# Performance work log

Measured on AMD Instinct MI355X. Metric: run time of the kernel, lower is better.

Reference implementation:

```python
import jax, jax.numpy as jnp
import numpy as np

N, D = 16384, 256
T = 0.5
C = 100


def setup_inputs() -> dict:
    key = jax.random.key(0)
    x = jax.random.normal(key, (N, D), dtype=jnp.float32)
    # L2-normalize rows (standard for contrastive embeddings; also keeps
    # exp(sim/T) in fp32 range, matching the module's intended use)
    x = x / jnp.linalg.norm(x, axis=1, keepdims=True)
    return {"x": x}


def reference(x) -> jnp.ndarray:
    # sim[i,j] = <x_i, x_j> / T ; loss = (1/C) * sum_i log(sum_j exp(sim[i,j]))
    sim = jnp.exp(jnp.matmul(x, x.T) / T)          # [N, N]
    row = jnp.log(jnp.sum(sim, axis=1))            # [N]
    return jnp.sum(row) / C                        # scalar
```

## Files before the change

kernel.cpp:

```cpp
#include <hip/hip_runtime.h>
#include <hip/hip_bf16.h>
#include <math.h>


#define N_ROWS 16384
#define KD     256
#define BM     256
#define BN     64
#define NT     (N_ROWS / BM)
#define NITER  (BM / BN)
#define NBLK   (NT * (NT + 1) / 2)

#define SCALE_SQRT 1.6986436f

typedef short short8 __attribute__((ext_vector_type(8)));
typedef float f32x4  __attribute__((ext_vector_type(4)));

typedef __attribute__((address_space(3))) void       lds_void;
typedef const __attribute__((address_space(1))) void gm_void;

__device__ __forceinline__ float fast_exp2(float x) {
#if __has_builtin(__builtin_amdgcn_exp2f)
    return __builtin_amdgcn_exp2f(x);
#else
    return exp2f(x);
#endif
}

__device__ __forceinline__ void gll16(const void* g, void* l) {
    __builtin_amdgcn_global_load_lds((gm_void*)g, (lds_void*)l, 16, 0, 0);
}

__global__ void convert_kernel(const float* __restrict__ x, unsigned short* __restrict__ xb,
                               float* __restrict__ out) {
    const int bx = blockIdx.x, tid = threadIdx.x;
    if (bx == 0 && tid == 0) out[0] = 0.f;
    int i = (bx * 256 + tid) * 4;
    float4 v = *(const float4*)(x + i);
    ushort4 o;
    {
        unsigned int u;
        u = __float_as_uint(v.x * SCALE_SQRT); u += 0x7fff + ((u >> 16) & 1); o.x = (unsigned short)(u >> 16);
        u = __float_as_uint(v.y * SCALE_SQRT); u += 0x7fff + ((u >> 16) & 1); o.y = (unsigned short)(u >> 16);
        u = __float_as_uint(v.z * SCALE_SQRT); u += 0x7fff + ((u >> 16) & 1); o.z = (unsigned short)(u >> 16);
        u = __float_as_uint(v.w * SCALE_SQRT); u += 0x7fff + ((u >> 16) & 1); o.w = (unsigned short)(u >> 16);
    }
    *(ushort4*)(xb + i) = o;
}

__global__ __launch_bounds__(256, 2)
void simloss_main(const unsigned short* __restrict__ xb, float* __restrict__ rowacc) {
    const int bid = blockIdx.x;
    int rb = (int)((sqrtf(8.f * (float)bid + 1.f) - 1.f) * 0.5f);
    while ((rb + 1) * (rb + 2) / 2 <= bid) ++rb;
    while (rb * (rb + 1) / 2 > bid) --rb;
    const int cb = bid - rb * (rb + 1) / 2;
    const bool diag = (rb == cb);

    __shared__ __align__(128) char smem[65536 + 1024 + 4096];
    float* const rowred = (float*)(smem + 65536);
    float* const colred = (float*)(smem + 65536 + 1024);

    const int tid  = threadIdx.x;
    const int lane = tid & 63;
    const int w    = tid >> 6;
    const int r0 = rb * BM;
    const int c0 = cb * BM;

    const int l15 = lane & 15;
    const int lg  = lane >> 4;

    short8 afrag[4][8];
    #pragma unroll
    for (int m = 0; m < 4; ++m) {
        const unsigned short* arow = xb + (size_t)(r0 + w * 64 + m * 16 + l15) * KD + lg * 8;
        #pragma unroll
        for (int kt = 0; kt < 8; ++kt)
            afrag[m][kt] = *(const short8*)(arow + kt * 32);
    }
    #pragma unroll
    for (int m = 0; m < 4; ++m)
        #pragma unroll
        for (int kt = 0; kt < 8; ++kt)
            asm volatile("" : "+v"(afrag[m][kt]));

    const unsigned short* bsrc0 = xb + (size_t)(c0 + w * 16 + l15) * KD + lg * 8;
    char* const ldst0 = smem + (w * 8) * 1024;

    auto stageB = [&](int buf, int it2) {
        const unsigned short* s = bsrc0 + (size_t)it2 * (BN * KD);
        char* dst = ldst0 + buf * 32768;
        #pragma unroll
        for (int kt = 0; kt < 8; ++kt)
            gll16(s + kt * 32, dst + kt * 1024);
    };

    float rowsum[4][4] = {{0.f}};

    stageB(0, 0);

    #pragma unroll 1
    for (int it = 0; it < NITER; ++it) {
        const int cur = it & 1;
        if (it + 1 < NITER) {
            stageB(cur ^ 1, it + 1);
            asm volatile("s_waitcnt vmcnt(8)" ::: "memory");
        } else {
            asm volatile("s_waitcnt vmcnt(0)" ::: "memory");
        }
        __builtin_amdgcn_s_barrier();
        asm volatile("" ::: "memory");

        const char* bbase = smem + cur * 32768;
        #pragma unroll
        for (int ct = 0; ct < 4; ++ct) {
            short8 bfrag[8];
            #pragma unroll
            for (int kt = 0; kt < 8; ++kt)
                bfrag[kt] = *(const short8*)(bbase + (ct * 8 + kt) * 1024 + lane * 16);
            f32x4 acc[4];
            #pragma unroll
            for (int m = 0; m < 4; ++m) acc[m] = (f32x4){0.f, 0.f, 0.f, 0.f};
            #pragma unroll
            for (int kt = 0; kt < 8; ++kt)
                #pragma unroll
                for (int m = 0; m < 4; ++m)
                    acc[m] = __builtin_amdgcn_mfma_f32_16x16x32_bf16(afrag[m][kt], bfrag[kt], acc[m], 0, 0, 0);
            float csum = 0.f;
            #pragma unroll
            for (int m = 0; m < 4; ++m)
                #pragma unroll
                for (int r = 0; r < 4; ++r) {
                    float e = fast_exp2(acc[m][r]);
                    rowsum[m][r] += e;
                    csum += e;
                }
            if (!diag) {
                csum += __shfl_xor(csum, 16);
                csum += __shfl_xor(csum, 32);
                if (lg == 0)
                    colred[w * 256 + it * 64 + ct * 16 + l15] = csum;
            }
        }

        asm volatile("" ::: "memory");
        __builtin_amdgcn_s_barrier();
        asm volatile("" ::: "memory");
    }

    #pragma unroll
    for (int m = 0; m < 4; ++m)
        #pragma unroll
        for (int r = 0; r < 4; ++r) {
            float v = rowsum[m][r];
            v += __shfl_xor(v, 1);
            v += __shfl_xor(v, 2);
            v += __shfl_xor(v, 4);
            v += __shfl_xor(v, 8);
            if (l15 == 0) rowred[w * 64 + m * 16 + lg * 4 + r] = v;
        }
    __syncthreads();

    rowacc[(size_t)cb * N_ROWS + r0 + tid] = rowred[tid];
    if (!diag) {
        float cs = colred[tid] + colred[256 + tid] + colred[512 + tid] + colred[768 + tid];
        rowacc[(size_t)rb * N_ROWS + c0 + tid] = cs;
    }
}

__global__ void finalize_kernel(const float* __restrict__ rowacc, float* __restrict__ out) {
    int i = blockIdx.x * 256 + threadIdx.x;
    float s = 0.f;
    #pragma unroll 8
    for (int k = 0; k < NT; ++k) s += rowacc[(size_t)k * N_ROWS + i];
    float v = logf(s);
    #pragma unroll
    for (int off = 1; off < 64; off <<= 1) v += __shfl_xor(v, off);
    __shared__ float red[4];
    if ((threadIdx.x & 63) == 0) red[threadIdx.x >> 6] = v;
    __syncthreads();
    if (threadIdx.x == 0)
        atomicAdd(out, (red[0] + red[1] + red[2] + red[3]) * 0.01f);
}

extern "C" void kernel_launch(void* const* d_in, const int* in_sizes, int n_in,
                              void* d_out, int out_size, void* d_ws, size_t ws_size,
                              hipStream_t stream) {
    const float* x = (const float*)d_in[0];
    unsigned short* xb = (unsigned short*)d_ws;
    float* rowacc = (float*)((char*)d_ws + (size_t)N_ROWS * KD * 2);
    float* out = (float*)d_out;

    convert_kernel<<<(N_ROWS * KD) / (256 * 4), 256, 0, stream>>>(x, xb, out);
    simloss_main<<<NBLK, 256, 0, stream>>>(xb, rowacc);
    finalize_kernel<<<N_ROWS / 256, 256, 0, stream>>>(rowacc, out);
}
```

Baseline: 162.9 us.

## Switch to persistent blocks walking contiguous tile ranges of the triangle

Instead of one block per 256x256 triangular tile, 512 blocks each take a contiguous range of about 8 tiles. Within a row-block a block keeps its A fragments in registers and streams column blocks through the double-buffered LDS pipeline. Column sums are written per tile, and partial row sums go to 32 extra per-block slots that convert_kernel now zeroes. The aim is a single even wave with no tail, fewer reloads of A, and less launch overhead. The cost is a longer finalize reduction (96 slots instead of 64) and more complex index bookkeeping.

```diff
diff --git a/kernel.cpp b/kernel.cpp
--- a/kernel.cpp
+++ b/kernel.cpp
@@ -5,11 +5,10 @@
 
 #define N_ROWS 16384
 #define KD     256
-#define BM     256
-#define BN     64
-#define NT     (N_ROWS / BM)
-#define NITER  (BM / BN)
-#define NBLK   (NT * (NT + 1) / 2)
+#define NT     64
+#define NTILE  (NT * (NT + 1) / 2)
+#define NBLK   512
+#define NSLOT  96
 
 #define SCALE_SQRT 1.6986436f
 
@@ -32,9 +31,11 @@
 }
 
 __global__ void convert_kernel(const float* __restrict__ x, unsigned short* __restrict__ xb,
-                               float* __restrict__ out) {
+                               float* __restrict__ rowacc, float* __restrict__ out) {
     const int bx = blockIdx.x, tid = threadIdx.x;
-    if (bx == 0 && tid == 0) out[0] = 0.f;
+    if (bx < (NSLOT * N_ROWS) / 1024)
+        *(float4*)(rowacc + (size_t)(bx * 256 + tid) * 4) = (float4){0.f, 0.f, 0.f, 0.f};
+    if (bx == 2000 && tid == 0) out[0] = 0.f;
     int i = (bx * 256 + tid) * 4;
     float4 v = *(const float4*)(x + i);
     ushort4 o;
@@ -50,13 +51,6 @@
 
 __global__ __launch_bounds__(256, 2)
 void simloss_main(const unsigned short* __restrict__ xb, float* __restrict__ rowacc) {
-    const int bid = blockIdx.x;
-    int rb = (int)((sqrtf(8.f * (float)bid + 1.f) - 1.f) * 0.5f);
-    while ((rb + 1) * (rb + 2) / 2 <= bid) ++rb;
-    while (rb * (rb + 1) / 2 > bid) --rb;
-    const int cb = bid - rb * (rb + 1) / 2;
-    const bool diag = (rb == cb);
-
     __shared__ __align__(128) char smem[65536 + 1024 + 4096];
     float* const rowred = (float*)(smem + 65536);
     float* const colred = (float*)(smem + 65536 + 1024);
@@ -64,107 +58,124 @@
     const int tid  = threadIdx.x;
     const int lane = tid & 63;
     const int w    = tid >> 6;
-    const int r0 = rb * BM;
-    const int c0 = cb * BM;
-
-    const int l15 = lane & 15;
-    const int lg  = lane >> 4;
-
-    short8 afrag[4][8];
-    #pragma unroll
-    for (int m = 0; m < 4; ++m) {
-        const unsigned short* arow = xb + (size_t)(r0 + w * 64 + m * 16 + l15) * KD + lg * 8;
+    const int l15  = lane & 15;
+    const int lg   = lane >> 4;
+    const int b    = blockIdx.x;
+
+    int t          = (b * 65) >> 4;
+    const int tEnd = ((b + 1) * 65) >> 4;
+    const int rowSlot = NT + (b & 31);
+
+    int rb = (int)((sqrtf(8.f * (float)t + 1.f) - 1.f) * 0.5f);
+    while ((rb + 1) * (rb + 2) / 2 <= t) ++rb;
+    while (rb * (rb + 1) / 2 > t) --rb;
+
+    #pragma unroll 1
+    while (t < tEnd) {
+        while ((rb + 1) * (rb + 2) / 2 <= t) ++rb;
+        const int rowStart = rb * (rb + 1) / 2;
+        const int cb0 = t - rowStart;
+        const int tE  = tEnd - rowStart;
+        const int cbE = tE < rb + 1 ? tE : rb + 1;
+        const int NI  = (cbE - cb0) * 4;
+        const int r0  = rb * 256;
+        const int colblk0 = cb0 * 4;
+
+        auto stageB = [&](int buf, int cblk) {
+            const unsigned short* s = xb + (size_t)(cblk * 64 + w * 16 + l15) * KD + lg * 8;
+            char* dst = smem + buf * 32768 + (w * 8) * 1024;
+            #pragma unroll
+            for (int kt = 0; kt < 8; ++kt)
+                gll16(s + kt * 32, dst + kt * 1024);
+        };
+        stageB(0, colblk0);
+
+        short8 afrag[4][8];
         #pragma unroll
-        for (int kt = 0; kt < 8; ++kt)
-            afrag[m][kt] = *(const short8*)(arow + kt * 32);
-    }
-    #pragma unroll
-    for (int m = 0; m < 4; ++m)
+        for (int m = 0; m < 4; ++m) {
+            const unsigned short* ar = xb + (size_t)(r0 + w * 64 + m * 16 + l15) * KD + lg * 8;
+            #pragma unroll
+            for (int kt = 0; kt < 8; ++kt)
+                afrag[m][kt] = *(const short8*)(ar + kt * 32);
+        }
         #pragma unroll
-        for (int kt = 0; kt < 8; ++kt)
-            asm volatile("" : "+v"(afrag[m][kt]));
-
-    const unsigned short* bsrc0 = xb + (size_t)(c0 + w * 16 + l15) * KD + lg * 8;
-    char* const ldst0 = smem + (w * 8) * 1024;
-
-    auto stageB = [&](int buf, int it2) {
-        const unsigned short* s = bsrc0 + (size_t)it2 * (BN * KD);
-        char* dst = ldst0 + buf * 32768;
-        #pragma unroll
-        for (int kt = 0; kt < 8; ++kt)
-            gll16(s + kt * 32, dst + kt * 1024);
-    };
-
-    float rowsum[4][4] = {{0.f}};
-
-    stageB(0, 0);
-
-    #pragma unroll 1
-    for (int it = 0; it < NITER; ++it) {
-        const int cur = it & 1;
-        if (it + 1 < NITER) {
-            stageB(cur ^ 1, it + 1);
-            asm volatile("s_waitcnt vmcnt(8)" ::: "memory");
-        } else {
-            asm volatile("s_waitcnt vmcnt(0)" ::: "memory");
-        }
-        __builtin_amdgcn_s_barrier();
-        asm volatile("" ::: "memory");
-
-        const char* bbase = smem + cur * 32768;
-        #pragma unroll
-        for (int ct = 0; ct < 4; ++ct) {
-            short8 bfrag[8];
+        for (int m = 0; m < 4; ++m)
             #pragma unroll
             for (int kt = 0; kt < 8; ++kt)
-                bfrag[kt] = *(const short8*)(bbase + (ct * 8 + kt) * 1024 + lane * 16);
-            f32x4 acc[4];
-            #pragma unroll
-            for (int m = 0; m < 4; ++m) acc[m] = (f32x4){0.f, 0.f, 0.f, 0.f};
-            #pragma unroll
-            for (int kt = 0; kt < 8; ++kt)
+                asm volatile("" : "+v"(afrag[m][kt]));
+
+        float rowsum[4][4] = {{0.f}};
+
+        #pragma unroll 1
+        for (int fi = 0; fi < NI; ++fi) {
+            const int cur = fi & 1;
+            if (fi + 1 < NI) {
+                stageB(cur ^ 1, colblk0 + fi + 1);
+                asm volatile("s_waitcnt vmcnt(8)" ::: "memory");
+            } else {
+                asm volatile("s_waitcnt vmcnt(0)" ::: "memory");
+            }
+            __builtin_amdgcn_s_barrier();
+            asm volatile("" ::: "memory");
+
+            const char* bbase = smem + cur * 32768;
+            #pragma unroll
+            for (int ct = 0; ct < 4; ++ct) {
+                short8 bfrag[8];
+                #pragma unroll
+                for (int kt = 0; kt < 8; ++kt)
+                    bfrag[kt] = *(const short8*)(bbase + (ct * 8 + kt) * 1024 + lane * 16);
+                f32x4 acc[4];
+                #pragma unroll
+                for (int m = 0; m < 4; ++m) acc[m] = (f32x4){0.f, 0.f, 0.f, 0.f};
+                #pragma unroll
+                for (int kt = 0; kt < 8; ++kt)
+                    #pragma unroll
+                    for (int m = 0; m < 4; ++m)
+                        acc[m] = __builtin_amdgcn_mfma_f32_16x16x32_bf16(afrag[m][kt], bfrag[kt], acc[m], 0, 0, 0);
+                float csum = 0.f;
                 #pragma unroll
                 for (int m = 0; m < 4; ++m)
-                    acc[m] = __builtin_amdgcn_mfma_f32_16x16x32_bf16(afrag[m][kt], bfrag[kt], acc[m], 0, 0, 0);
-            float csum = 0.f;
-            #pragma unroll
-            for (int m = 0; m < 4; ++m)
-                #pragma unroll
-                for (int r = 0; r < 4; ++r) {
-                    float e = fast_exp2(acc[m][r]);
-                    rowsum[m][r] += e;
-                    csum += e;
-                }
-            if (!diag) {
+                    #pragma unroll
+                    for (int r = 0; r < 4; ++r) {
+                        float e = fast_exp2(acc[m][r]);
+                        rowsum[m][r] += e;
+                        csum += e;
+                    }
                 csum += __shfl_xor(csum, 16);
                 csum += __shfl_xor(csum, 32);
                 if (lg == 0)
-                    colred[w * 256 + it * 64 + ct * 16 + l15] = csum;
+                    colred[w * 256 + (fi & 3) * 64 + ct * 16 + l15] = csum;
+            }
+
+            asm volatile("" ::: "memory");
+            __builtin_amdgcn_s_barrier();
+            asm volatile("" ::: "memory");
+
+            if ((fi & 3) == 3) {
+                const int cb = cb0 + (fi >> 2);
+                if (cb != rb) {
+                    float cs = colred[tid] + colred[256 + tid] + colred[512 + tid] + colred[768 + tid];
+                    rowacc[(size_t)rb * N_ROWS + cb * 256 + tid] = cs;
+                }
             }
         }
 
-        asm volatile("" ::: "memory");
-        __builtin_amdgcn_s_barrier();
-        asm volatile("" ::: "memory");
-    }
-
-    #pragma unroll
-    for (int m = 0; m < 4; ++m)
         #pragma unroll
-        for (int r = 0; r < 4; ++r) {
-            float v = rowsum[m][r];
-            v += __shfl_xor(v, 1);
-            v += __shfl_xor(v, 2);
-            v += __shfl_xor(v, 4);
-            v += __shfl_xor(v, 8);
-            if (l15 == 0) rowred[w * 64 + m * 16 + lg * 4 + r] = v;
-        }
-    __syncthreads();
-
-    rowacc[(size_t)cb * N_ROWS + r0 + tid] = rowred[tid];
-    if (!diag) {
-        float cs = colred[tid] + colred[256 + tid] + colred[512 + tid] + colred[768 + tid];
-        rowacc[(size_t)rb * N_ROWS + c0 + tid] = cs;
+        for (int m = 0; m < 4; ++m)
+            #pragma unroll
+            for (int r = 0; r < 4; ++r) {
+                float v = rowsum[m][r];
+                v += __shfl_xor(v, 1);
+                v += __shfl_xor(v, 2);
+                v += __shfl_xor(v, 4);
+                v += __shfl_xor(v, 8);
+                if (l15 == 0) rowred[w * 64 + m * 16 + lg * 4 + r] = v;
+            }
+        __syncthreads();
+        rowacc[(size_t)rowSlot * N_ROWS + r0 + tid] = rowred[tid];
+
+        t = rowStart + cbE;
     }
 }
 
@@ -172,7 +183,7 @@
     int i = blockIdx.x * 256 + threadIdx.x;
     float s = 0.f;
     #pragma unroll 8
-    for (int k = 0; k < NT; ++k) s += rowacc[(size_t)k * N_ROWS + i];
+    for (int k = 0; k < NSLOT; ++k) s += rowacc[(size_t)k * N_ROWS + i];
     float v = logf(s);
     #pragma unroll
     for (int off = 1; off < 64; off <<= 1) v += __shfl_xor(v, off);
@@ -191,7 +202,7 @@
     float* rowacc = (float*)((char*)d_ws + (size_t)N_ROWS * KD * 2);
     float* out = (float*)d_out;
 
-    convert_kernel<<<(N_ROWS * KD) / (256 * 4), 256, 0, stream>>>(x, xb, out);
+    convert_kernel<<<(N_ROWS * KD) / (256 * 4), 256, 0, stream>>>(x, xb, rowacc, out);
     simloss_main<<<NBLK, 256, 0, stream>>>(xb, rowacc);
     finalize_kernel<<<N_ROWS / 256, 256, 0, stream>>>(rowacc, out);
 }
```

Result: faster. 149.9 us (-8.0%).
